# Kernel tuning notes

Measured on AMD Instinct MI355X. Metric: run time of the kernel, lower is better.

Reference implementation:

```python
import jax, jax.numpy as jnp
import numpy as np

B, N, C, H = 2, 2048, 1024, 16
D = C // H          # head dim = 64
HID = 4 * C         # MLP hidden = 4096
LN_EPS = 1e-5
ROPE_BASE = 10000.0


def layernorm(x, g, b):
    mu = jnp.mean(x, axis=-1, keepdims=True)
    var = jnp.var(x, axis=-1, keepdims=True)
    return (x - mu) * jax.lax.rsqrt(var + LN_EPS) * g + b


def rotate_half(x):
    # interleaved pairs: (x0, x1) -> (-x1, x0), lucidrains rotary_embedding_torch style
    x = x.reshape(*x.shape[:-1], -1, 2)
    x1, x2 = x[..., 0], x[..., 1]
    return jnp.stack([-x2, x1], axis=-1).reshape(*x.shape[:-2], -1)


def rope_cos_sin(n, d, dtype):
    inv_freq = 1.0 / (ROPE_BASE ** (jnp.arange(0, d, 2, dtype=jnp.float32) / d))
    ang = jnp.arange(n, dtype=jnp.float32)[:, None] * inv_freq          # [N, D/2]
    ang = jnp.repeat(ang, 2, axis=-1)                                    # [N, D] interleaved
    return jnp.cos(ang).astype(dtype), jnp.sin(ang).astype(dtype)


def setup_inputs() -> dict:
    key = jax.random.key(0)
    ks = jax.random.split(key, 16)
    s = 0.02
    return {
        "x": jax.random.normal(ks[0], (B, N, C), jnp.float32),
        "ln1_g": jnp.ones((C,), jnp.float32),
        "ln1_b": jnp.zeros((C,), jnp.float32),
        "qkv_w": jax.random.normal(ks[1], (C, 3 * C), jnp.float32) * s,   # stored [in, out]
        "qkv_b": jnp.zeros((3 * C,), jnp.float32),
        "proj_w": jax.random.normal(ks[2], (C, C), jnp.float32) * s,
        "proj_b": jnp.zeros((C,), jnp.float32),
        "ln2_g": jnp.ones((C,), jnp.float32),
        "ln2_b": jnp.zeros((C,), jnp.float32),
        "fc1_w": jax.random.normal(ks[3], (C, HID), jnp.float32) * s,
        "fc1_b": jnp.zeros((HID,), jnp.float32),
        "ffn_ln_g": jnp.ones((HID,), jnp.float32),
        "ffn_ln_b": jnp.zeros((HID,), jnp.float32),
        "fc2_w": jax.random.normal(ks[4], (HID, C), jnp.float32) * s,
        "fc2_b": jnp.zeros((C,), jnp.float32),
    }


def reference(x, ln1_g, ln1_b, qkv_w, qkv_b, proj_w, proj_b,
              ln2_g, ln2_b, fc1_w, fc1_b, ffn_ln_g, ffn_ln_b, fc2_w, fc2_b):
    b, n, c = x.shape
    h, d = H, c // H
    scale = d ** -0.5

    # --- attention branch (pre-norm) ---
    hx = layernorm(x, ln1_g, ln1_b)
    qkv = hx @ qkv_w + qkv_b                                   # [B,N,3C]
    qkv = qkv.reshape(b, n, 3, h, d).transpose(2, 0, 3, 1, 4)  # [3,B,H,N,D]
    q, k, v = qkv[0], qkv[1], qkv[2]

    cos, sin = rope_cos_sin(n, d, x.dtype)                     # [N,D]
    q = q * cos + rotate_half(q) * sin
    k = k * cos + rotate_half(k) * sin

    attn = jax.nn.softmax(jnp.einsum('bhqd,bhkd->bhqk', q, k) * scale, axis=-1)
    o = jnp.einsum('bhqk,bhkd->bhqd', attn, v)                 # [B,H,N,D]
    o = o.transpose(0, 2, 1, 3).reshape(b, n, c)               # B N (H D)
    x = x + o @ proj_w + proj_b

    # --- MLP branch (pre-norm; GELU then LayerNorm on hidden, per FeedForwardBlock) ---
    m = layernorm(x, ln2_g, ln2_b)
    m = jax.nn.gelu(m @ fc1_w + fc1_b, approximate=False)
    m = layernorm(m, ffn_ln_g, ffn_ln_b)
    m = m @ fc2_w + fc2_b
    return x + m
```

## Files before the change

kernel.cpp:

```cpp
#include <hip/hip_runtime.h>
#include <hip/hip_bf16.h>
#include <cmath>

typedef __bf16 bf16_t;
typedef __bf16 bf16x8 __attribute__((ext_vector_type(8)));
typedef float f32x4 __attribute__((ext_vector_type(4)));
typedef float f32x16 __attribute__((ext_vector_type(16)));
typedef unsigned short u16;
typedef unsigned int u32;

#if defined(__has_builtin)
#if __has_builtin(__builtin_amdgcn_exp2f)
#define ATTN_EXP(x) __builtin_amdgcn_exp2f(x)
#define ATTN_LOG2E 1.4426950408889634f
#endif
#endif
#ifndef ATTN_EXP
#define ATTN_EXP(x) __expf(x)
#define ATTN_LOG2E 1.0f
#endif

__device__ __forceinline__ void load16(const bf16_t* g, bf16_t* l) {
  __builtin_amdgcn_global_load_lds((const __attribute__((address_space(1))) u32*)g,
                                   (__attribute__((address_space(3))) u32*)l, 16, 0, 0);
}

__device__ __forceinline__ u32 pk2(float a, float b) {
  bf16_t x = (bf16_t)a, y = (bf16_t)b;
  u16 ux = __builtin_bit_cast(u16, x), uy = __builtin_bit_cast(u16, y);
  return (u32)ux | ((u32)uy << 16);
}

union V4U { u32 w[4]; bf16x8 v; };

__device__ __forceinline__ void tr32(const float* __restrict__ src, bf16_t* __restrict__ dst,
                                     int Kd, int Nd, int ntile, int ktile, int tid) {
  __shared__ float tile[32][33];
  int n0 = ntile * 32, k0 = ktile * 32;
  int tx = tid & 31, ty = tid >> 5;
  for (int i = ty; i < 32; i += 8)
    tile[i][tx] = src[(size_t)(k0 + i) * Nd + n0 + tx];
  __syncthreads();
  for (int i = ty; i < 32; i += 8)
    dst[(size_t)(n0 + i) * Kd + k0 + tx] = (bf16_t)tile[tx][i];
}

__global__ __launch_bounds__(256) void prep_kernel(
    const float* __restrict__ qkv_w, const float* __restrict__ proj_w,
    const float* __restrict__ fc1_w, const float* __restrict__ fc2_w,
    bf16_t* __restrict__ qkvT, bf16_t* __restrict__ projT,
    bf16_t* __restrict__ fc1T, bf16_t* __restrict__ fc2T,
    float* __restrict__ ropeC, float* __restrict__ ropeS) {
  int b = blockIdx.x, tid = threadIdx.x;
  if (b < 3072) {
    tr32(qkv_w, qkvT, 1024, 3072, b % 96, b / 96, tid);
  } else if (b < 4096) {
    int r = b - 3072; tr32(proj_w, projT, 1024, 1024, r % 32, r / 32, tid);
  } else if (b < 8192) {
    int r = b - 4096; tr32(fc1_w, fc1T, 1024, 4096, r % 128, r / 128, tid);
  } else if (b < 12288) {
    int r = b - 8192; tr32(fc2_w, fc2T, 4096, 1024, r % 32, r / 32, tid);
  } else {
    int idx = (b - 12288) * 256 + tid;
    int pos = idx >> 5, t = idx & 31;
    float e = (float)(2 * t) / 64.0f;
    float inv = powf(10000.0f, -e);
    float a = (float)pos * inv;
    ropeC[idx] = cosf(a);
    ropeS[idx] = sinf(a);
  }
}

template <typename TI, int W>
__global__ __launch_bounds__(256) void ln_kernel(const TI* __restrict__ in,
                                                 const float* __restrict__ g,
                                                 const float* __restrict__ b,
                                                 bf16_t* __restrict__ out) {
  constexpr int PT = W / 256;
  int row = blockIdx.x;
  const TI* p = in + (size_t)row * W;
  float vals[PT];
  float s = 0.f, q = 0.f;
  for (int i = 0; i < PT; ++i) {
    float v = (float)p[threadIdx.x + i * 256];
    vals[i] = v; s += v; q += v * v;
  }
  for (int off = 32; off; off >>= 1) { s += __shfl_xor(s, off); q += __shfl_xor(q, off); }
  __shared__ float red[8];
  int wave = threadIdx.x >> 6, lane = threadIdx.x & 63;
  if (lane == 0) { red[wave] = s; red[4 + wave] = q; }
  __syncthreads();
  s = red[0] + red[1] + red[2] + red[3];
  q = red[4] + red[5] + red[6] + red[7];
  float mu = s * (1.0f / W);
  float var = q * (1.0f / W) - mu * mu;
  float rstd = rsqrtf(var + 1e-5f);
  bf16_t* op = out + (size_t)row * W;
  for (int i = 0; i < PT; ++i) {
    int cix = threadIdx.x + i * 256;
    op[cix] = (bf16_t)((vals[i] - mu) * rstd * g[cix] + b[cix]);
  }
}

enum { EPI_QKV = 0, EPI_RESID = 1, EPI_GELU = 2 };

template <int EPI>
__global__ __launch_bounds__(256, 2) void gemm_bt(
    const bf16_t* __restrict__ A, const bf16_t* __restrict__ Bt, int M, int Nn, int K,
    const float* __restrict__ bias, const float* __restrict__ resid,
    float* __restrict__ outf, bf16_t* __restrict__ outb,
    bf16_t* __restrict__ qb, bf16_t* __restrict__ kb, bf16_t* __restrict__ vtb,
    const float* __restrict__ ropeC, const float* __restrict__ ropeS) {
  __shared__ bf16_t lsA[128 * 32];
  __shared__ bf16_t lsB[128 * 32];
  const int tid = threadIdx.x;
  const int lane = tid & 63;
  const int wave = tid >> 6;
  const int l16 = lane & 15, quad = lane >> 4;
  const int wm = (wave >> 1) * 64, wn = (wave & 1) * 64;
  const int m0 = blockIdx.y * 128, n0 = blockIdx.x * 128;

  f32x4 acc[4][4];
  for (int i = 0; i < 4; ++i)
    for (int j = 0; j < 4; ++j) acc[i][j] = {0.f, 0.f, 0.f, 0.f};

  for (int kk = 0; kk < K; kk += 32) {
    __syncthreads();
    for (int i = 0; i < 2; ++i) {
      int s = tid + i * 256;
      int row = s >> 2, ch = s & 3;
      load16(A + (size_t)(m0 + row) * K + kk + ch * 8, lsA + s * 8);
      load16(Bt + (size_t)(n0 + row) * K + kk + ch * 8, lsB + s * 8);
    }
    __syncthreads();
    bf16x8 af[4], bfr[4];
    for (int t = 0; t < 4; ++t) {
      af[t] = *(const bf16x8*)(lsA + (wm + t * 16 + l16) * 32 + quad * 8);
      bfr[t] = *(const bf16x8*)(lsB + (wn + t * 16 + l16) * 32 + quad * 8);
    }
    for (int mt = 0; mt < 4; ++mt)
      for (int nt = 0; nt < 4; ++nt)
        acc[mt][nt] = __builtin_amdgcn_mfma_f32_16x16x32_bf16(af[mt], bfr[nt], acc[mt][nt], 0, 0, 0);
  }

  for (int mt = 0; mt < 4; ++mt) {
    for (int nt = 0; nt < 4; ++nt) {
      int gn = n0 + wn + nt * 16 + l16;
      int gm0 = m0 + wm + mt * 16 + quad * 4;
      if constexpr (EPI == EPI_QKV) {
        int which = gn >> 10;
        int hd = gn & 1023, head = hd >> 6, d = hd & 63;
        if (which == 2) {
          u32 lo, hi;
          {
            float v0 = acc[mt][nt][0] + bias[gn];
            float v1 = acc[mt][nt][1] + bias[gn];
            float v2 = acc[mt][nt][2] + bias[gn];
            float v3 = acc[mt][nt][3] + bias[gn];
            lo = pk2(v0, v1);
            hi = pk2(v2, v3);
          }
          int b = gm0 >> 11, pos = gm0 & 2047;
          int bh = b * 16 + head;
          uint2 pk; pk.x = lo; pk.y = hi;
          *(uint2*)(vtb + ((size_t)bh * 64 + d) * 2048 + pos) = pk;
        } else {
          bf16_t* dst = (which == 0) ? qb : kb;
          int t = d >> 1;
          for (int r = 0; r < 4; ++r) {
            float v = acc[mt][nt][r] + bias[gn];
            float pn = __shfl_xor(v, 1);
            int gm = gm0 + r;
            int b = gm >> 11, pos = gm & 2047;
            float cc = ropeC[pos * 32 + t], ss = ropeS[pos * 32 + t];
            float o = (d & 1) ? (v * cc + pn * ss) : (v * cc - pn * ss);
            dst[(((size_t)(b * 16 + head)) * 2048 + pos) * 64 + d] = (bf16_t)o;
          }
        }
      } else if constexpr (EPI == EPI_GELU) {
        for (int r = 0; r < 4; ++r) {
          int gm = gm0 + r;
          float v = acc[mt][nt][r] + bias[gn];
          float g = 0.5f * v * (1.0f + erff(v * 0.70710678118654752f));
          outb[(size_t)gm * Nn + gn] = (bf16_t)g;
        }
      } else {
        for (int r = 0; r < 4; ++r) {
          int gm = gm0 + r;
          size_t idx = (size_t)gm * Nn + gn;
          outf[idx] = acc[mt][nt][r] + bias[gn] + resid[idx];
        }
      }
    }
  }
}

__global__ __launch_bounds__(256, 2) void attn_kernel(
    const bf16_t* __restrict__ q, const bf16_t* __restrict__ k,
    const bf16_t* __restrict__ vt, bf16_t* __restrict__ o) {
  __shared__ bf16_t lsK[2][128 * 64];
  __shared__ bf16_t lsV[2][64 * 128];

  const int tid = threadIdx.x, lane = tid & 63, wave = tid >> 6;
  const int c31 = lane & 31, hi = lane >> 5, h7 = c31 & 7;
  const int bh = blockIdx.y, qt = blockIdx.x;
  const int b = bh >> 4, h = bh & 15;
  const bf16_t* qp = q + (size_t)bh * 2048 * 64;
  const bf16_t* kp = k + (size_t)bh * 2048 * 64;
  const bf16_t* vp = vt + (size_t)bh * 64 * 2048;
  const int qrow0 = qt * 128 + wave * 32;
  const int qrow = qrow0 + c31;

  const float QS = 0.125f * ATTN_LOG2E;
  bf16x8 qb[4];
#pragma unroll
  for (int ks = 0; ks < 4; ++ks) {
    bf16x8 t = *(const bf16x8*)(qp + (size_t)qrow * 64 + ks * 16 + hi * 8);
#pragma unroll
    for (int j = 0; j < 8; ++j) t[j] = (bf16_t)((float)t[j] * QS);
    qb[ks] = t;
  }

  f32x16 oacc[2];
  oacc[0] = 0.f; oacc[1] = 0.f;
  float mstate = -3.0e38f, lstate = 0.f;

  auto stage = [&](int kt, int buf) {
    const bf16_t* kg = kp + (size_t)kt * 128 * 64;
    bf16_t* lk = &lsK[buf][0];
    bf16_t* lv = &lsV[buf][0];
#pragma unroll
    for (int i = 0; i < 4; ++i) {
      int s = tid + i * 256;
      int kr = s >> 3, kc = (s & 7) ^ (kr & 7);
      load16(kg + (size_t)kr * 64 + kc * 8, lk + s * 8);
      int vr = s >> 4, vc = (s & 15) ^ (vr & 7);
      load16(vp + (size_t)vr * 2048 + kt * 128 + vc * 8, lv + s * 8);
    }
  };

  stage(0, 0);
  for (int kt = 0; kt < 16; ++kt) {
    __syncthreads();
    if (kt < 15) stage(kt + 1, (kt + 1) & 1);
    const bf16_t* lk = &lsK[kt & 1][0];
    const bf16_t* lv = &lsV[kt & 1][0];

    f32x16 sacc[4];
    sacc[0] = 0.f; sacc[1] = 0.f; sacc[2] = 0.f; sacc[3] = 0.f;
#pragma unroll
    for (int ks = 0; ks < 4; ++ks) {
      int cs = ((ks * 2 + hi) ^ h7) * 8;
#pragma unroll
      for (int nt = 0; nt < 4; ++nt) {
        bf16x8 kf = *(const bf16x8*)(lk + (nt * 32 + c31) * 64 + cs);
        sacc[nt] = __builtin_amdgcn_mfma_f32_32x32x16_bf16(kf, qb[ks], sacc[nt], 0, 0, 0);
      }
    }

    float mx = sacc[0][0];
#pragma unroll
    for (int nt = 0; nt < 4; ++nt)
#pragma unroll
      for (int r = 0; r < 16; ++r) mx = fmaxf(mx, sacc[nt][r]);
    mx = fmaxf(mx, __shfl_xor(mx, 32));
    float mnew = fmaxf(mstate, mx);
    float alpha = ATTN_EXP(mstate - mnew);
    mstate = mnew;
    float rs = 0.f;
    u32 u[4][4][2];
#pragma unroll
    for (int nt = 0; nt < 4; ++nt)
#pragma unroll
      for (int t = 0; t < 4; ++t) {
        float p0 = ATTN_EXP(sacc[nt][4 * t + 0] - mnew);
        float p1 = ATTN_EXP(sacc[nt][4 * t + 1] - mnew);
        float p2 = ATTN_EXP(sacc[nt][4 * t + 2] - mnew);
        float p3 = ATTN_EXP(sacc[nt][4 * t + 3] - mnew);
        rs += (p0 + p1) + (p2 + p3);
        u[nt][t][0] = pk2(p0, p1);
        u[nt][t][1] = pk2(p2, p3);
      }
    rs += __shfl_xor(rs, 32);
    lstate = lstate * alpha + rs;
#pragma unroll
    for (int dt = 0; dt < 2; ++dt)
#pragma unroll
      for (int r = 0; r < 16; ++r) oacc[dt][r] *= alpha;

#pragma unroll
    for (int ks = 0; ks < 8; ++ks) {
      int n = ks >> 1, t0 = (ks & 1) * 2;
      u32 a0 = u[n][t0][0], a1 = u[n][t0][1];
      u32 b0 = u[n][t0 + 1][0], b1 = u[n][t0 + 1][1];
      u32 ax0 = (u32)__shfl_xor((int)a0, 32), ax1 = (u32)__shfl_xor((int)a1, 32);
      u32 bx0 = (u32)__shfl_xor((int)b0, 32), bx1 = (u32)__shfl_xor((int)b1, 32);
      V4U f;
      f.w[0] = hi ? bx0 : a0;
      f.w[1] = hi ? bx1 : a1;
      f.w[2] = hi ? b0 : ax0;
      f.w[3] = hi ? b1 : ax1;
      bf16x8 pf = f.v;
      int cs = ((ks * 2 + hi) ^ h7) * 8;
#pragma unroll
      for (int dt = 0; dt < 2; ++dt) {
        bf16x8 vf = *(const bf16x8*)(lv + (dt * 32 + c31) * 128 + cs);
        oacc[dt] = __builtin_amdgcn_mfma_f32_32x32x16_bf16(vf, pf, oacc[dt], 0, 0, 0);
      }
    }
  }

  float inv = 1.0f / lstate;
  bf16_t* orow = o + ((size_t)(b * 2048 + qrow)) * 1024 + h * 64;
#pragma unroll
  for (int dt = 0; dt < 2; ++dt)
#pragma unroll
    for (int t = 0; t < 4; ++t) {
      int d0 = dt * 32 + 8 * t + 4 * hi;
      uint2 pk;
      pk.x = pk2(oacc[dt][4 * t + 0] * inv, oacc[dt][4 * t + 1] * inv);
      pk.y = pk2(oacc[dt][4 * t + 2] * inv, oacc[dt][4 * t + 3] * inv);
      *(uint2*)(orow + d0) = pk;
    }
}

extern "C" void kernel_launch(void* const* d_in, const int* in_sizes, int n_in,
                              void* d_out, int out_size, void* d_ws, size_t ws_size,
                              hipStream_t stream) {
  const float* x = (const float*)d_in[0];
  const float* ln1_g = (const float*)d_in[1];
  const float* ln1_b = (const float*)d_in[2];
  const float* qkv_w = (const float*)d_in[3];
  const float* qkv_b = (const float*)d_in[4];
  const float* proj_w = (const float*)d_in[5];
  const float* proj_b = (const float*)d_in[6];
  const float* ln2_g = (const float*)d_in[7];
  const float* ln2_b = (const float*)d_in[8];
  const float* fc1_w = (const float*)d_in[9];
  const float* fc1_b = (const float*)d_in[10];
  const float* ffg = (const float*)d_in[11];
  const float* ffb = (const float*)d_in[12];
  const float* fc2_w = (const float*)d_in[13];
  const float* fc2_b = (const float*)d_in[14];
  float* out = (float*)d_out;

  char* ws = (char*)d_ws;
  size_t off = 0;
  auto alloc = [&](size_t n) { char* p = ws + off; off += (n + 255) & ~(size_t)255; return p; };

  bf16_t* qkvT  = (bf16_t*)alloc(3072ull * 1024 * 2);
  bf16_t* projT = (bf16_t*)alloc(1024ull * 1024 * 2);
  bf16_t* fc1T  = (bf16_t*)alloc(4096ull * 1024 * 2);
  bf16_t* fc2T  = (bf16_t*)alloc(1024ull * 4096 * 2);
  float*  ropeC = (float*)alloc(2048ull * 32 * 4);
  float*  ropeS = (float*)alloc(2048ull * 32 * 4);
  bf16_t* hx    = (bf16_t*)alloc(4096ull * 1024 * 2);
  bf16_t* qbuf  = (bf16_t*)alloc(32ull * 2048 * 64 * 2);
  bf16_t* kbuf  = (bf16_t*)alloc(32ull * 2048 * 64 * 2);
  bf16_t* vtbuf = (bf16_t*)alloc(32ull * 64 * 2048 * 2);
  bf16_t* obuf  = (bf16_t*)alloc(4096ull * 1024 * 2);
  float*  x2    = (float*)alloc(4096ull * 1024 * 4);
  bf16_t* h1    = (bf16_t*)alloc(4096ull * 4096 * 2);
  bf16_t* hln   = (bf16_t*)qbuf;

  prep_kernel<<<12544, 256, 0, stream>>>(qkv_w, proj_w, fc1_w, fc2_w,
                                         qkvT, projT, fc1T, fc2T, ropeC, ropeS);

  ln_kernel<float, 1024><<<4096, 256, 0, stream>>>(x, ln1_g, ln1_b, hx);
  gemm_bt<EPI_QKV><<<dim3(24, 32), 256, 0, stream>>>(hx, qkvT, 4096, 3072, 1024, qkv_b,
      nullptr, nullptr, nullptr, qbuf, kbuf, vtbuf, ropeC, ropeS);
  attn_kernel<<<dim3(16, 32), 256, 0, stream>>>(qbuf, kbuf, vtbuf, obuf);
  gemm_bt<EPI_RESID><<<dim3(8, 32), 256, 0, stream>>>(obuf, projT, 4096, 1024, 1024, proj_b,
      x, x2, nullptr, nullptr, nullptr, nullptr, nullptr, nullptr);
  ln_kernel<float, 1024><<<4096, 256, 0, stream>>>(x2, ln2_g, ln2_b, hx);
  gemm_bt<EPI_GELU><<<dim3(32, 32), 256, 0, stream>>>(hx, fc1T, 4096, 4096, 1024, fc1_b,
      nullptr, nullptr, h1, nullptr, nullptr, nullptr, nullptr, nullptr);
  ln_kernel<bf16_t, 4096><<<4096, 256, 0, stream>>>(h1, ffg, ffb, hln);
  gemm_bt<EPI_RESID><<<dim3(8, 32), 256, 0, stream>>>(hln, fc2T, 4096, 1024, 4096, fc2_b,
      x2, out, nullptr, nullptr, nullptr, nullptr, nullptr, nullptr);
}
```

Baseline: 416.5 us.

## Double-buffer GEMM LDS tiles, XOR-swizzle LDS layout, use 64-row tiles for N=1024 GEMMs

The GEMM kernel now stages the next K-slice into a second LDS buffer while the current one is consumed, so a single barrier per iteration replaces the load-then-compute serialization. LDS chunk placement is XOR-swizzled by row to reduce bank conflicts on the fragment reads. A TM template parameter lets the proj and fc2 GEMMs use 64-row tiles with twice as many blocks, improving CU occupancy for the narrow outputs. The costs are double the LDS footprint and lower per-block reuse on the smaller tiles.

```diff
diff --git a/kernel.cpp b/kernel.cpp
--- a/kernel.cpp
+++ b/kernel.cpp
@@ -104,46 +104,70 @@
 
 enum { EPI_QKV = 0, EPI_RESID = 1, EPI_GELU = 2 };
 
-template <int EPI>
+template <int EPI, int TM>
 __global__ __launch_bounds__(256, 2) void gemm_bt(
     const bf16_t* __restrict__ A, const bf16_t* __restrict__ Bt, int M, int Nn, int K,
     const float* __restrict__ bias, const float* __restrict__ resid,
     float* __restrict__ outf, bf16_t* __restrict__ outb,
     bf16_t* __restrict__ qb, bf16_t* __restrict__ kb, bf16_t* __restrict__ vtb,
     const float* __restrict__ ropeC, const float* __restrict__ ropeS) {
-  __shared__ bf16_t lsA[128 * 32];
-  __shared__ bf16_t lsB[128 * 32];
+  constexpr int MT = TM / 32;
+  __shared__ bf16_t lsA[2][TM * 32];
+  __shared__ bf16_t lsB[2][128 * 32];
   const int tid = threadIdx.x;
   const int lane = tid & 63;
   const int wave = tid >> 6;
   const int l16 = lane & 15, quad = lane >> 4;
-  const int wm = (wave >> 1) * 64, wn = (wave & 1) * 64;
-  const int m0 = blockIdx.y * 128, n0 = blockIdx.x * 128;
-
-  f32x4 acc[4][4];
-  for (int i = 0; i < 4; ++i)
+  const int wm = (wave >> 1) * (TM / 2), wn = (wave & 1) * 64;
+  const int m0 = blockIdx.y * TM, n0 = blockIdx.x * 128;
+
+  f32x4 acc[MT][4];
+  for (int i = 0; i < MT; ++i)
     for (int j = 0; j < 4; ++j) acc[i][j] = {0.f, 0.f, 0.f, 0.f};
 
-  for (int kk = 0; kk < K; kk += 32) {
-    __syncthreads();
+  auto stage = [&](int kk, int buf) {
+    bf16_t* la = &lsA[buf][0];
+    bf16_t* lb = &lsB[buf][0];
+#pragma unroll
+    for (int i = 0; i < TM / 64; ++i) {
+      int s = tid + i * 256;
+      int row = s >> 2, ch = (s & 3) ^ (row & 3);
+      load16(A + (size_t)(m0 + row) * K + kk + ch * 8, la + s * 8);
+    }
+#pragma unroll
     for (int i = 0; i < 2; ++i) {
       int s = tid + i * 256;
-      int row = s >> 2, ch = s & 3;
-      load16(A + (size_t)(m0 + row) * K + kk + ch * 8, lsA + s * 8);
-      load16(Bt + (size_t)(n0 + row) * K + kk + ch * 8, lsB + s * 8);
-    }
+      int row = s >> 2, ch = (s & 3) ^ (row & 3);
+      load16(Bt + (size_t)(n0 + row) * K + kk + ch * 8, lb + s * 8);
+    }
+  };
+
+  const int nk = K >> 5;
+  stage(0, 0);
+  for (int ki = 0; ki < nk; ++ki) {
     __syncthreads();
-    bf16x8 af[4], bfr[4];
+    if (ki + 1 < nk) stage((ki + 1) << 5, (ki + 1) & 1);
+    const bf16_t* la = &lsA[ki & 1][0];
+    const bf16_t* lb = &lsB[ki & 1][0];
+    bf16x8 af[MT], bfr[4];
+#pragma unroll
+    for (int t = 0; t < MT; ++t) {
+      int row = wm + t * 16 + l16;
+      af[t] = *(const bf16x8*)(la + row * 32 + (quad ^ (row & 3)) * 8);
+    }
+#pragma unroll
     for (int t = 0; t < 4; ++t) {
-      af[t] = *(const bf16x8*)(lsA + (wm + t * 16 + l16) * 32 + quad * 8);
-      bfr[t] = *(const bf16x8*)(lsB + (wn + t * 16 + l16) * 32 + quad * 8);
-    }
-    for (int mt = 0; mt < 4; ++mt)
+      int row = wn + t * 16 + l16;
+      bfr[t] = *(const bf16x8*)(lb + row * 32 + (quad ^ (row & 3)) * 8);
+    }
+#pragma unroll
+    for (int mt = 0; mt < MT; ++mt)
+#pragma unroll
       for (int nt = 0; nt < 4; ++nt)
         acc[mt][nt] = __builtin_amdgcn_mfma_f32_16x16x32_bf16(af[mt], bfr[nt], acc[mt][nt], 0, 0, 0);
   }
 
-  for (int mt = 0; mt < 4; ++mt) {
+  for (int mt = 0; mt < MT; ++mt) {
     for (int nt = 0; nt < 4; ++nt) {
       int gn = n0 + wn + nt * 16 + l16;
       int gm0 = m0 + wm + mt * 16 + quad * 4;
@@ -367,15 +391,15 @@
                                          qkvT, projT, fc1T, fc2T, ropeC, ropeS);
 
   ln_kernel<float, 1024><<<4096, 256, 0, stream>>>(x, ln1_g, ln1_b, hx);
-  gemm_bt<EPI_QKV><<<dim3(24, 32), 256, 0, stream>>>(hx, qkvT, 4096, 3072, 1024, qkv_b,
+  gemm_bt<EPI_QKV, 128><<<dim3(24, 32), 256, 0, stream>>>(hx, qkvT, 4096, 3072, 1024, qkv_b,
       nullptr, nullptr, nullptr, qbuf, kbuf, vtbuf, ropeC, ropeS);
   attn_kernel<<<dim3(16, 32), 256, 0, stream>>>(qbuf, kbuf, vtbuf, obuf);
-  gemm_bt<EPI_RESID><<<dim3(8, 32), 256, 0, stream>>>(obuf, projT, 4096, 1024, 1024, proj_b,
+  gemm_bt<EPI_RESID, 64><<<dim3(8, 64), 256, 0, stream>>>(obuf, projT, 4096, 1024, 1024, proj_b,
       x, x2, nullptr, nullptr, nullptr, nullptr, nullptr, nullptr);
   ln_kernel<float, 1024><<<4096, 256, 0, stream>>>(x2, ln2_g, ln2_b, hx);
-  gemm_bt<EPI_GELU><<<dim3(32, 32), 256, 0, stream>>>(hx, fc1T, 4096, 4096, 1024, fc1_b,
+  gemm_bt<EPI_GELU, 128><<<dim3(32, 32), 256, 0, stream>>>(hx, fc1T, 4096, 4096, 1024, fc1_b,
       nullptr, nullptr, h1, nullptr, nullptr, nullptr, nullptr, nullptr);
   ln_kernel<bf16_t, 4096><<<4096, 256, 0, stream>>>(h1, ffg, ffb, hln);
-  gemm_bt<EPI_RESID><<<dim3(8, 32), 256, 0, stream>>>(hln, fc2T, 4096, 1024, 4096, fc2_b,
+  gemm_bt<EPI_RESID, 64><<<dim3(8, 64), 256, 0, stream>>>(hln, fc2T, 4096, 1024, 4096, fc2_b,
       x2, out, nullptr, nullptr, nullptr, nullptr, nullptr, nullptr);
 }
```

Result: faster. 398.5 us (-4.3%).
